# Optimization experiments

Hardware: AMD Instinct MI355X
Metric: run time of the kernel (lower is better)

## Reference

```python
import jax, jax.numpy as jnp
import numpy as np

EPS = 1.1920929e-07  # torch RMSNorm default eps = finfo(float32).eps

def rmsnorm(x, w):
    return x * jax.lax.rsqrt(jnp.mean(x * x, axis=-1, keepdims=True) + EPS) * w

def setup_inputs() -> dict:
    key = jax.random.key(0)
    ks = jax.random.split(key, 12)
    D, H, SC, ST = 1024, 16, 64, 16
    B, T = 2, 2048
    s = 0.02
    return {
        "x": jax.random.normal(ks[0], (B, T, D), jnp.float32),
        "qkv_w": jax.random.normal(ks[1], (3 * D, D), jnp.float32) * s,
        "o_w": jax.random.normal(ks[2], (D, D), jnp.float32) * s,
        "norm1_w": jnp.ones((D,), jnp.float32),
        "norm2_w": jnp.ones((D,), jnp.float32),
        "in_w": jax.random.normal(ks[3], (SC, D), jnp.float32) * s,
        "out_w": jax.random.normal(ks[4], (D, SC), jnp.float32) * s,  # zeros in torch init; randn for nontrivial baseline
        "A_log": jax.random.normal(ks[5], (SC, ST), jnp.float32) * 0.1,
        "Bp_w": jax.random.normal(ks[6], (ST, SC), jnp.float32) * s,
        "Cp_w": jax.random.normal(ks[7], (ST, SC), jnp.float32) * s,
        "dt_w": jax.random.normal(ks[8], (SC, SC), jnp.float32) * s,
        "dt_b": jnp.full((SC,), -3.0, jnp.float32),
        "gate_w": jax.random.normal(ks[9], (SC, D), jnp.float32) * s,
    }

def selective_scan(h, in_w, out_w, A_log, Bp_w, Cp_w, dt_w, dt_b, gate_w):
    B, T, D = h.shape
    SC, ST = A_log.shape
    z = h @ in_w.T                      # [B,T,SC]
    gate = jax.nn.silu(h @ gate_w.T)    # [B,T,SC]
    A = -jnp.exp(A_log)                 # [SC,ST]
    Bi = z @ Bp_w.T                     # [B,T,ST]
    Ci = z @ Cp_w.T                     # [B,T,ST]
    dt = jax.nn.softplus(z @ dt_w.T + dt_b)  # [B,T,SC]
    A_bar = 1.0 + dt[..., None] * A     # [B,T,SC,ST]

    def step(state, inp):
        a_bar, dtz_t, b_t, c_t = inp    # [B,SC,ST],[B,SC],[B,ST],[B,ST]
        state = a_bar * state + dtz_t[:, :, None] * b_t[:, None, :]
        y = jnp.sum(state * c_t[:, None, :], axis=-1)  # [B,SC]
        return state, y

    init = jnp.zeros((B, SC, ST), h.dtype)
    xs = (jnp.swapaxes(A_bar, 0, 1), jnp.swapaxes(dt * z, 0, 1),
          jnp.swapaxes(Bi, 0, 1), jnp.swapaxes(Ci, 0, 1))
    _, ys = jax.lax.scan(step, init, xs)      # [T,B,SC]
    y = jnp.swapaxes(ys, 0, 1) * gate         # [B,T,SC]
    return y @ out_w.T                        # [B,T,D]

def reference(x, qkv_w, o_w, norm1_w, norm2_w, in_w, out_w, A_log, Bp_w, Cp_w, dt_w, dt_b, gate_w):
    B, T, D = x.shape
    H = 16
    hd = D // H
    h = rmsnorm(x, norm1_w)
    qkv = (h @ qkv_w.T).reshape(B, T, 3, H, hd)
    qkv = jnp.transpose(qkv, (2, 0, 3, 1, 4))  # [3,B,H,T,hd]
    q, k, v = qkv[0], qkv[1], qkv[2]
    attn = jnp.einsum('bhqd,bhkd->bhqk', q, k) / np.sqrt(hd).astype(np.float32)
    mask = jnp.tril(jnp.ones((T, T), bool))
    attn = jnp.where(mask, attn, -jnp.inf)
    attn = jax.nn.softmax(attn, axis=-1)
    out = jnp.einsum('bhqk,bhkd->bhqd', attn, v)
    out = jnp.transpose(out, (0, 2, 1, 3)).reshape(B, T, D)
    x = x + out @ o_w.T
    h2 = rmsnorm(x, norm2_w)
    x = x + selective_scan(h2, in_w, out_w, A_log, Bp_w, Cp_w, dt_w, dt_b, gate_w)
    return x
```

## Files before the change

kernel.cpp:

```cpp
#include <hip/hip_runtime.h>
#include <hip/hip_bf16.h>
#include <math.h>

typedef __hip_bfloat16 bf16;
typedef __attribute__((ext_vector_type(4))) float v_f32x4;
typedef __attribute__((ext_vector_type(4))) unsigned short v_u16x4;
typedef __attribute__((ext_vector_type(8))) unsigned short v_u16x8;
typedef __attribute__((ext_vector_type(8))) __bf16 v_bf16x8;
typedef __attribute__((ext_vector_type(4))) __bf16 v_bf16x4;
typedef __attribute__((ext_vector_type(4))) short v_s16x4;

#define NB 2
#define NT 2048
#define ND 1024
#define NH 16
#define NSC 64
#define NST 16
#define NM (NB*NT)
#define RMS_EPS 1.1920929e-07f
#define NCHUNK 32
#define CLEN 64

__device__ inline float b2f(unsigned short u) {
  union { unsigned int i; float f; } v; v.i = ((unsigned int)u) << 16; return v.f;
}
__device__ inline unsigned short f2b(float f) {
  union { float f; unsigned int i; } v; v.f = f;
  unsigned int r = (v.i + 0x7FFF + ((v.i >> 16) & 1)) >> 16;
  return (unsigned short)r;
}

__device__ inline v_f32x4 mfma16(v_bf16x4 a, v_bf16x4 b, v_f32x4 c) {
#if __has_builtin(__builtin_amdgcn_mfma_f32_16x16x16_bf16)
  return __builtin_amdgcn_mfma_f32_16x16x16_bf16(a, b, c, 0, 0, 0);
#else
  union U { v_bf16x4 h; v_s16x4 s; };
  U ua, ub; ua.h = a; ub.h = b;
  return __builtin_amdgcn_mfma_f32_16x16x16bf16_1k(ua.s, ub.s, c, 0, 0, 0);
#endif
}

__device__ inline void gl_lds16(const bf16* g, bf16* l) {
  __builtin_amdgcn_global_load_lds((__attribute__((address_space(1))) void*)g,
                                   (__attribute__((address_space(3))) void*)l,
                                   16, 0, 0);
}

__global__ __launch_bounds__(256) void cvt_rms_kernel(
    const float* __restrict__ qkv_w, const float* __restrict__ o_w,
    const float* __restrict__ out_w, const float* __restrict__ in_w,
    const float* __restrict__ gate_w, const float* __restrict__ dt_w,
    const float* __restrict__ Bp_w, const float* __restrict__ Cp_w,
    bf16* __restrict__ qkvw_b, bf16* __restrict__ ow_b, bf16* __restrict__ outw_b,
    bf16* __restrict__ W1, bf16* __restrict__ W2,
    const float* __restrict__ x, const float* __restrict__ n1w, bf16* __restrict__ h) {
  const int blk = blockIdx.x, t = threadIdx.x;
  if (blk >= 4295) {
    const int row = blk - 4295;
    v_f32x4 xv = *(const v_f32x4*)(x + (size_t)row * ND + t * 4);
    float s = xv[0]*xv[0] + xv[1]*xv[1] + xv[2]*xv[2] + xv[3]*xv[3];
    #pragma unroll
    for (int off = 32; off; off >>= 1) s += __shfl_xor(s, off, 64);
    __shared__ float red[4];
    __shared__ float scale_s;
    if ((t & 63) == 0) red[t >> 6] = s;
    __syncthreads();
    if (t == 0) scale_s = rsqrtf((red[0] + red[1] + red[2] + red[3]) * (1.0f / ND) + RMS_EPS);
    __syncthreads();
    float sc = scale_s;
    v_f32x4 wv = *(const v_f32x4*)(n1w + t * 4);
    v_u16x4 o;
    o[0] = f2b(xv[0] * sc * wv[0]);
    o[1] = f2b(xv[1] * sc * wv[1]);
    o[2] = f2b(xv[2] * sc * wv[2]);
    o[3] = f2b(xv[3] * sc * wv[3]);
    *(v_u16x4*)((unsigned short*)h + (size_t)row * ND + t * 4) = o;
    return;
  }
  const float* src; bf16* dst; int base;
  if (blk < 3072)      { src = qkv_w;  dst = qkvw_b;      base = blk; }
  else if (blk < 4096) { src = o_w;    dst = ow_b;        base = blk - 3072; }
  else if (blk < 4160) { src = out_w;  dst = outw_b;      base = blk - 4096; }
  else if (blk < 4224) { src = in_w;   dst = W1;          base = blk - 4160; }
  else if (blk < 4288) { src = gate_w; dst = W1 + 65536;  base = blk - 4224; }
  else if (blk < 4292) { src = dt_w;   dst = W2;          base = blk - 4288; }
  else if (blk == 4292){ src = Bp_w;   dst = W2 + 4096;   base = 0; }
  else if (blk == 4293){ src = Cp_w;   dst = W2 + 5120;   base = 0; }
  else {
    v_u16x8 z;
    #pragma unroll
    for (int i = 0; i < 8; i++) z[i] = 0;
    *(v_u16x8*)(W2 + 6144 + t * 8) = z;
    return;
  }
  int i = base * 256 + t;
  v_f32x4 v = ((const v_f32x4*)src)[i];
  v_u16x4 o;
  o[0] = f2b(v[0]); o[1] = f2b(v[1]); o[2] = f2b(v[2]); o[3] = f2b(v[3]);
  ((v_u16x4*)dst)[i] = o;
}

template <bool RES, bool OUTF32, bool VT>
__global__ __launch_bounds__(256) void gemm_bt_kernel(
    const bf16* __restrict__ A, const bf16* __restrict__ Bw,
    const float* __restrict__ res, void* __restrict__ Cout, int N, int K, int lda,
    bf16* __restrict__ VtG) {
  __shared__ alignas(16) bf16 As[128 * 32];
  __shared__ alignas(16) bf16 Bs[128 * 32];
  const int tid = threadIdx.x;
  const int wid = tid >> 6;
  const int lane = tid & 63;
  const int c = lane & 15;
  const int quad = lane >> 4;
  const int m0 = blockIdx.y * 128;
  const int n0 = blockIdx.x * 128;
  const int wm = (wid >> 1) * 64;
  const int wn = (wid & 1) * 64;
  const int srow = tid >> 2;
  const int schunk = tid & 3;

  const bf16* Ap0 = A + (size_t)(m0 + srow) * lda + schunk * 8;
  const bf16* Ap1 = Ap0 + (size_t)64 * lda;
  const bf16* Bp0 = Bw + (size_t)(n0 + srow) * K + schunk * 8;
  const bf16* Bp1 = Bp0 + (size_t)64 * K;
  bf16* AsW0 = As + wid * 512;
  bf16* AsW1 = As + 2048 + wid * 512;
  bf16* BsW0 = Bs + wid * 512;
  bf16* BsW1 = Bs + 2048 + wid * 512;

  v_f32x4 acc[4][4];
  #pragma unroll
  for (int i = 0; i < 4; i++)
    #pragma unroll
    for (int j = 0; j < 4; j++)
      #pragma unroll
      for (int r = 0; r < 4; r++) acc[i][j][r] = 0.0f;

  const int nk = K >> 5;
  for (int kt = 0; kt < nk; kt++) {
    gl_lds16(Ap0 + kt * 32, AsW0);
    gl_lds16(Ap1 + kt * 32, AsW1);
    gl_lds16(Bp0 + kt * 32, BsW0);
    gl_lds16(Bp1 + kt * 32, BsW1);
    __syncthreads();
    v_bf16x8 af[4], bfw[4];
    #pragma unroll
    for (int i = 0; i < 4; i++)
      af[i] = *(const v_bf16x8*)&As[(wm + i * 16 + c) * 32 + quad * 8];
    #pragma unroll
    for (int j = 0; j < 4; j++)
      bfw[j] = *(const v_bf16x8*)&Bs[(wn + j * 16 + c) * 32 + quad * 8];
    #pragma unroll
    for (int i = 0; i < 4; i++)
      #pragma unroll
      for (int j = 0; j < 4; j++)
        acc[i][j] = __builtin_amdgcn_mfma_f32_16x16x32_bf16(af[i], bfw[j], acc[i][j], 0, 0, 0);
    __syncthreads();
  }

  if (VT && n0 >= 2048) {
    #pragma unroll
    for (int i = 0; i < 4; i++)
      #pragma unroll
      for (int j = 0; j < 4; j++) {
        int hcol = n0 + wn + j * 16 + c - 2048;
        int hh = hcol >> 6, dd = hcol & 63;
        int rg0 = m0 + wm + i * 16 + quad * 4;
        int bb = rg0 >> 11, t0 = rg0 & (NT - 1);
        v_u16x4 ov;
        #pragma unroll
        for (int r = 0; r < 4; r++) ov[r] = f2b(acc[i][j][r]);
        *(v_u16x4*)((unsigned short*)VtG + ((size_t)((bb * NH + hh) * 64 + dd)) * NT + t0) = ov;
      }
    return;
  }

  #pragma unroll
  for (int i = 0; i < 4; i++)
    #pragma unroll
    for (int j = 0; j < 4; j++)
      #pragma unroll
      for (int r = 0; r < 4; r++) {
        int rg = m0 + wm + i * 16 + quad * 4 + r;
        int cg = n0 + wn + j * 16 + c;
        size_t idx = (size_t)rg * N + cg;
        float v = acc[i][j][r];
        if (RES) v += res[idx];
        if (OUTF32) ((float*)Cout)[idx] = v;
        else ((bf16*)Cout)[idx] = __float2bfloat16(v);
      }
}

template <bool RES, bool OUTF32>
__global__ __launch_bounds__(256) void gemm_bt64_kernel(
    const bf16* __restrict__ A, const bf16* __restrict__ Bw,
    const float* __restrict__ res, void* __restrict__ Cout, int N, int K, int lda) {
  __shared__ alignas(16) bf16 As[64 * 32];
  __shared__ alignas(16) bf16 Bs[128 * 32];
  const int tid = threadIdx.x;
  const int wid = tid >> 6;
  const int lane = tid & 63;
  const int c = lane & 15;
  const int quad = lane >> 4;
  const int m0 = blockIdx.y * 64;
  const int n0 = blockIdx.x * 128;
  const int wm = (wid & 1) * 32;
  const int wn = (wid >> 1) * 64;
  const int srow = tid >> 2;
  const int schunk = tid & 3;

  const bf16* Ap = A + (size_t)(m0 + srow) * lda + schunk * 8;
  const bf16* Bp0 = Bw + (size_t)(n0 + srow) * K + schunk * 8;
  const bf16* Bp1 = Bp0 + (size_t)64 * K;
  bf16* AsW  = As + wid * 512;
  bf16* BsW0 = Bs + wid * 512;
  bf16* BsW1 = Bs + 2048 + wid * 512;

  v_f32x4 acc[2][4];
  #pragma unroll
  for (int i = 0; i < 2; i++)
    #pragma unroll
    for (int j = 0; j < 4; j++)
      #pragma unroll
      for (int r = 0; r < 4; r++) acc[i][j][r] = 0.0f;

  const int nk = K >> 5;
  for (int kt = 0; kt < nk; kt++) {
    gl_lds16(Ap + kt * 32, AsW);
    gl_lds16(Bp0 + kt * 32, BsW0);
    gl_lds16(Bp1 + kt * 32, BsW1);
    __syncthreads();
    v_bf16x8 af[2], bfw[4];
    #pragma unroll
    for (int i = 0; i < 2; i++)
      af[i] = *(const v_bf16x8*)&As[(wm + i * 16 + c) * 32 + quad * 8];
    #pragma unroll
    for (int j = 0; j < 4; j++)
      bfw[j] = *(const v_bf16x8*)&Bs[(wn + j * 16 + c) * 32 + quad * 8];
    #pragma unroll
    for (int i = 0; i < 2; i++)
      #pragma unroll
      for (int j = 0; j < 4; j++)
        acc[i][j] = __builtin_amdgcn_mfma_f32_16x16x32_bf16(af[i], bfw[j], acc[i][j], 0, 0, 0);
    __syncthreads();
  }

  #pragma unroll
  for (int i = 0; i < 2; i++)
    #pragma unroll
    for (int j = 0; j < 4; j++)
      #pragma unroll
      for (int r = 0; r < 4; r++) {
        int rg = m0 + wm + i * 16 + quad * 4 + r;
        int cg = n0 + wn + j * 16 + c;
        size_t idx = (size_t)rg * N + cg;
        float v = acc[i][j][r];
        if (RES) v += res[idx];
        if (OUTF32) ((float*)Cout)[idx] = v;
        else ((bf16*)Cout)[idx] = __float2bfloat16(v);
      }
}

__global__ __launch_bounds__(256) void attn_kernel(const bf16* __restrict__ qkv,
                                                   const bf16* __restrict__ VtG,
                                                   bf16* __restrict__ OP,
                                                   float* __restrict__ L) {
  __shared__ alignas(16) bf16 Qs[64 * 72];
  __shared__ alignas(16) bf16 Ks[64 * 72];
  __shared__ alignas(16) bf16 Vt[64 * 72];
  const int tid = threadIdx.x;
  const int w = tid >> 6;
  const int lane = tid & 63;
  const int c = lane & 15;
  const int quad = lane >> 4;
  const int id = blockIdx.x;
  const int bh = id & 31;
  const int u = id >> 5;
  const int half = u >> 5;
  const int v = u & 31;
  const int j0 = v & 7;
  const int qt = (v & 24) | (((v >> 3) & 1) ? (7 - j0) : j0);
  const int b = bh >> 4;
  const int h = bh & 15;
  const int srow = tid >> 2;
  const int schunk = tid & 3;
  const int n = qt + 1;
  const int nh0 = (n + 1) >> 1;
  const int k0 = half ? nh0 : 0;
  const int k1 = half ? n : nh0;

  {
    const bf16* src = qkv + (size_t)(b * NT + qt * 64 + srow) * 3072 + h * 64 + schunk * 16;
    *(v_u16x8*)&Qs[srow * 72 + schunk * 16] = *(const v_u16x8*)src;
    *(v_u16x8*)&Qs[srow * 72 + schunk * 16 + 8] = *(const v_u16x8*)(src + 8);
  }
  __syncthreads();
  v_bf16x8 aq0 = *(const v_bf16x8*)&Qs[(w * 16 + c) * 72 + quad * 8];
  v_bf16x8 aq1 = *(const v_bf16x8*)&Qs[(w * 16 + c) * 72 + 32 + quad * 8];

  float l_part = 0.0f;
  v_f32x4 o[4];
  #pragma unroll
  for (int jd = 0; jd < 4; jd++)
    #pragma unroll
    for (int r = 0; r < 4; r++) o[jd][r] = 0.0f;

  const int qrow = w * 16 + c;

  for (int kt = k0; kt < k1; kt++) {
    {
      const bf16* ksrc = qkv + (size_t)(b * NT + kt * 64 + srow) * 3072 + 1024 + h * 64 + schunk * 16;
      *(v_u16x8*)&Ks[srow * 72 + schunk * 16] = *(const v_u16x8*)ksrc;
      *(v_u16x8*)&Ks[srow * 72 + schunk * 16 + 8] = *(const v_u16x8*)(ksrc + 8);
      const bf16* vsrc = VtG + (size_t)(bh * 64 + srow) * NT + kt * 64 + schunk * 16;
      *(v_u16x8*)&Vt[srow * 72 + schunk * 16] = *(const v_u16x8*)vsrc;
      *(v_u16x8*)&Vt[srow * 72 + schunk * 16 + 8] = *(const v_u16x8*)(vsrc + 8);
    }
    __syncthreads();

    const bool diag = (kt == qt);
    v_bf16x4 pf[4];
    #pragma unroll
    for (int j = 0; j < 4; j++) {
      v_bf16x8 ak0 = *(const v_bf16x8*)&Ks[(j * 16 + c) * 72 + quad * 8];
      v_bf16x8 ak1 = *(const v_bf16x8*)&Ks[(j * 16 + c) * 72 + 32 + quad * 8];
      v_f32x4 z;
      #pragma unroll
      for (int r = 0; r < 4; r++) z[r] = 0.0f;
      z = __builtin_amdgcn_mfma_f32_16x16x32_bf16(ak0, aq0, z, 0, 0, 0);
      z = __builtin_amdgcn_mfma_f32_16x16x32_bf16(ak1, aq1, z, 0, 0, 0);
      v_u16x4 pu;
      #pragma unroll
      for (int r = 0; r < 4; r++) {
        float p = __expf(z[r] * 0.125f);
        if (diag && (j * 16 + quad * 4 + r) > qrow) p = 0.0f;
        l_part += p;
        pu[r] = f2b(p);
      }
      union { v_u16x4 u; v_bf16x4 h; } cv; cv.u = pu;
      pf[j] = cv.h;
    }
    #pragma unroll
    for (int jd = 0; jd < 4; jd++)
      #pragma unroll
      for (int j = 0; j < 4; j++) {
        v_bf16x4 av = *(const v_bf16x4*)&Vt[(jd * 16 + c) * 72 + j * 16 + quad * 4];
        o[jd] = mfma16(av, pf[j], o[jd]);
      }
    __syncthreads();
  }

  float l = l_part;
  l += __shfl_xor(l, 16, 64);
  l += __shfl_xor(l, 32, 64);

  const size_t ti = (size_t)((bh * 32 + qt) * 2 + half);
  if (quad == 0) L[ti * 64 + qrow] = l;
  unsigned short* OPu = (unsigned short*)OP + (ti * 64 + qrow) * 64;
  #pragma unroll
  for (int jd = 0; jd < 4; jd++) {
    v_u16x4 ov;
    #pragma unroll
    for (int r = 0; r < 4; r++) ov[r] = f2b(o[jd][r]);
    *(v_u16x4*)(OPu + jd * 16 + quad * 4) = ov;
  }
}

__global__ __launch_bounds__(256) void attn_combine_kernel(
    const bf16* __restrict__ OP, const float* __restrict__ L, bf16* __restrict__ out) {
  const int bq = blockIdx.x;
  const int bh = bq >> 5, qt = bq & 31;
  const int b = bh >> 4, h = bh & 15;
  const int tid = threadIdx.x;
  const int q = tid >> 2, dg = (tid & 3) * 16;
  const size_t ti0 = (size_t)bq * 2;
  float inv = 1.0f / (L[ti0 * 64 + q] + L[(ti0 + 1) * 64 + q]);
  const unsigned short* O0 = (const unsigned short*)OP + (ti0 * 64 + q) * 64 + dg;
  const unsigned short* O1 = (const unsigned short*)OP + ((ti0 + 1) * 64 + q) * 64 + dg;
  unsigned short* dst = (unsigned short*)out + (size_t)(b * NT + qt * 64 + q) * ND + h * 64 + dg;
  #pragma unroll
  for (int i = 0; i < 16; i += 4) {
    v_u16x4 a = *(const v_u16x4*)(O0 + i);
    v_u16x4 bb = *(const v_u16x4*)(O1 + i);
    v_u16x4 o;
    #pragma unroll
    for (int r = 0; r < 4; r++) o[r] = f2b((b2f(a[r]) + b2f(bb[r])) * inv);
    *(v_u16x4*)(dst + i) = o;
  }
}

__global__ __launch_bounds__(256) void proj_scan_kernel(
    const float* __restrict__ x1, const float* __restrict__ n2w,
    const bf16* __restrict__ W1, const bf16* __restrict__ W2,
    const float* __restrict__ dt_b,
    float* __restrict__ dt_a, float* __restrict__ dtz_a,
    float* __restrict__ gate_a, float* __restrict__ P2) {
  __shared__ alignas(16) bf16 h2S[16 * 1032];
  __shared__ alignas(16) bf16 Bs[128 * 32];
  __shared__ alignas(16) bf16 zgS[16 * 136];
  const int tid = threadIdx.x;
  const int w = tid >> 6, lane = tid & 63, c = lane & 15, quad = lane >> 4;
  const int m0 = blockIdx.x * 16;
  unsigned short* h2Su = (unsigned short*)h2S;
  unsigned short* zgSu = (unsigned short*)zgS;

  {
    const int r16 = tid >> 4, ct = tid & 15;
    const float* xr = x1 + (size_t)(m0 + r16) * ND + ct * 64;
    v_f32x4 xv[16];
    float ss = 0.0f;
    #pragma unroll
    for (int i = 0; i < 16; i++) {
      xv[i] = *(const v_f32x4*)(xr + i * 4);
      ss += xv[i][0]*xv[i][0] + xv[i][1]*xv[i][1] + xv[i][2]*xv[i][2] + xv[i][3]*xv[i][3];
    }
    ss += __shfl_xor(ss, 1, 64);
    ss += __shfl_xor(ss, 2, 64);
    ss += __shfl_xor(ss, 4, 64);
    ss += __shfl_xor(ss, 8, 64);
    float sc = rsqrtf(ss * (1.0f / ND) + RMS_EPS);
    const float* wr = n2w + ct * 64;
    #pragma unroll
    for (int i = 0; i < 16; i++) {
      v_f32x4 wv = *(const v_f32x4*)(wr + i * 4);
      v_u16x4 o;
      o[0] = f2b(xv[i][0] * sc * wv[0]);
      o[1] = f2b(xv[i][1] * sc * wv[1]);
      o[2] = f2b(xv[i][2] * sc * wv[2]);
      o[3] = f2b(xv[i][3] * sc * wv[3]);
      *(v_u16x4*)&h2Su[r16 * 1032 + ct * 64 + i * 4] = o;
    }
  }
  __syncthreads();

  const int lrow = lane >> 2, lk = lane & 3;
  v_f32x4 acc[2];
  #pragma unroll
  for (int j = 0; j < 2; j++)
    #pragma unroll
    for (int r = 0; r < 4; r++) acc[j][r] = 0.0f;
  for (int kt = 0; kt < 32; kt++) {
    gl_lds16(W1 + (size_t)(w * 32 + lrow) * 1024 + kt * 32 + lk * 8, Bs + (w * 32) * 32);
    gl_lds16(W1 + (size_t)(w * 32 + 16 + lrow) * 1024 + kt * 32 + lk * 8, Bs + (w * 32 + 16) * 32);
    __syncthreads();
    v_bf16x8 af = *(const v_bf16x8*)&h2S[c * 1032 + kt * 32 + quad * 8];
    #pragma unroll
    for (int j = 0; j < 2; j++) {
      v_bf16x8 bfw = *(const v_bf16x8*)&Bs[(w * 32 + j * 16 + c) * 32 + quad * 8];
      acc[j] = __builtin_amdgcn_mfma_f32_16x16x32_bf16(af, bfw, acc[j], 0, 0, 0);
    }
    __syncthreads();
  }
  #pragma unroll
  for (int j = 0; j < 2; j++)
    #pragma unroll
    for (int r = 0; r < 4; r++)
      zgSu[(quad * 4 + r) * 136 + w * 32 + j * 16 + c] = f2b(acc[j][r]);
  __syncthreads();

  v_f32x4 acc2[2];
  #pragma unroll
  for (int j = 0; j < 2; j++)
    #pragma unroll
    for (int r = 0; r < 4; r++) acc2[j][r] = 0.0f;
  for (int kt = 0; kt < 2; kt++) {
    gl_lds16(W2 + (size_t)(w * 32 + lrow) * 64 + kt * 32 + lk * 8, Bs + (w * 32) * 32);
    gl_lds16(W2 + (size_t)(w * 32 + 16 + lrow) * 64 + kt * 32 + lk * 8, Bs + (w * 32 + 16) * 32);
    __syncthreads();
    v_bf16x8 af = *(const v_bf16x8*)&zgS[c * 136 + kt * 32 + quad * 8];
    #pragma unroll
    for (int j = 0; j < 2; j++) {
      v_bf16x8 bfw = *(const v_bf16x8*)&Bs[(w * 32 + j * 16 + c) * 32 + quad * 8];
      acc2[j] = __builtin_amdgcn_mfma_f32_16x16x32_bf16(af, bfw, acc2[j], 0, 0, 0);
    }
    __syncthreads();
  }

  #pragma unroll
  for (int j = 0; j < 2; j++)
    #pragma unroll
    for (int r = 0; r < 4; r++) {
      const int row = quad * 4 + r;
      const int col = w * 32 + j * 16 + c;
      const size_t grow = (size_t)(m0 + row);
      if (w < 2) {
        float z = b2f(zgSu[row * 136 + col]);
        float a = acc2[j][r] + dt_b[col];
        float dt = (a > 20.0f) ? a : log1pf(__expf(a));
        dt_a[grow * NSC + col] = dt;
        dtz_a[grow * NSC + col] = dt * z;
      } else {
        P2[grow * 128 + col] = acc2[j][r];
        float g = b2f(zgSu[row * 136 + col]);
        gate_a[grow * NSC + (col - 64)] = g / (1.0f + __expf(-g));
      }
    }
}

__global__ __launch_bounds__(256) void scanA_kernel(
    const float* __restrict__ dt_a, const float* __restrict__ dtz_a,
    const float* __restrict__ P2, const float* __restrict__ A_log,
    float* __restrict__ Pbuf, float* __restrict__ Sbuf) {
  __shared__ float dtS[CLEN * 16], dtzS[CLEN * 16], biS[CLEN * 16];
  const int k = blockIdx.x, scg = blockIdx.y, b = blockIdx.z;
  const int tid = threadIdx.x;
  const int t0 = k * CLEN;
  {
    int r = tid >> 2, c4 = (tid & 3) * 4;
    *(v_f32x4*)&dtS[r * 16 + c4]  = *(const v_f32x4*)&dt_a[(size_t)(b * NT + t0 + r) * NSC + scg * 16 + c4];
    *(v_f32x4*)&dtzS[r * 16 + c4] = *(const v_f32x4*)&dtz_a[(size_t)(b * NT + t0 + r) * NSC + scg * 16 + c4];
    *(v_f32x4*)&biS[r * 16 + c4]  = *(const v_f32x4*)&P2[(size_t)(b * NT + t0 + r) * 128 + 64 + c4];
  }
  __syncthreads();
  const int st = tid & 15, scl = tid >> 4;
  const float A = -__expf(A_log[(scg * 16 + scl) * NST + st]);
  float P = 1.0f, s = 0.0f;
  #pragma unroll
  for (int t = 0; t < CLEN; t++) {
    float a = fmaf(dtS[t * 16 + scl], A, 1.0f);
    float u = dtzS[t * 16 + scl] * biS[t * 16 + st];
    P *= a;
    s = fmaf(a, s, u);
  }
  size_t idx = (size_t)(b * NCHUNK + k) * 1024 + scg * 256 + tid;
  Pbuf[idx] = P;
  Sbuf[idx] = s;
}

__global__ __launch_bounds__(256) void scanC_kernel(
    const float* __restrict__ dt_a, const float* __restrict__ dtz_a,
    const float* __restrict__ P2, const float* __restrict__ gate_a,
    const float* __restrict__ A_log, const float* __restrict__ Pbuf,
    const float* __restrict__ Sbuf, bf16* __restrict__ ys) {
  __shared__ float dtS[CLEN * 16], dtzS[CLEN * 16], biS[CLEN * 16], ciS[CLEN * 16], gS[CLEN * 16];
  const int k = blockIdx.x, scg = blockIdx.y, b = blockIdx.z;
  const int tid = threadIdx.x;
  const int t0 = k * CLEN;
  {
    int r = tid >> 2, c4 = (tid & 3) * 4;
    *(v_f32x4*)&dtS[r * 16 + c4]  = *(const v_f32x4*)&dt_a[(size_t)(b * NT + t0 + r) * NSC + scg * 16 + c4];
    *(v_f32x4*)&dtzS[r * 16 + c4] = *(const v_f32x4*)&dtz_a[(size_t)(b * NT + t0 + r) * NSC + scg * 16 + c4];
    *(v_f32x4*)&biS[r * 16 + c4]  = *(const v_f32x4*)&P2[(size_t)(b * NT + t0 + r) * 128 + 64 + c4];
    *(v_f32x4*)&ciS[r * 16 + c4]  = *(const v_f32x4*)&P2[(size_t)(b * NT + t0 + r) * 128 + 80 + c4];
    *(v_f32x4*)&gS[r * 16 + c4]   = *(const v_f32x4*)&gate_a[(size_t)(b * NT + t0 + r) * NSC + scg * 16 + c4];
  }
  const int st = tid & 15, scl = tid >> 4;
  const float A = -__expf(A_log[(scg * 16 + scl) * NST + st]);
  float s = 0.0f;
  for (int kk = 0; kk < k; kk++) {
    size_t idx = (size_t)(b * NCHUNK + kk) * 1024 + scg * 256 + tid;
    s = fmaf(Pbuf[idx], s, Sbuf[idx]);
  }
  __syncthreads();
  for (int t = 0; t < CLEN; t++) {
    float a = fmaf(dtS[t * 16 + scl], A, 1.0f);
    float u = dtzS[t * 16 + scl] * biS[t * 16 + st];
    s = fmaf(a, s, u);
    float pv = s * ciS[t * 16 + st];
    pv += __shfl_xor(pv, 1, 64);
    pv += __shfl_xor(pv, 2, 64);
    pv += __shfl_xor(pv, 4, 64);
    pv += __shfl_xor(pv, 8, 64);
    if (st == 0)
      ys[(size_t)(b * NT + t0 + t) * NSC + scg * 16 + scl] = __float2bfloat16(pv * gS[t * 16 + scl]);
  }
}

extern "C" void kernel_launch(void* const* d_in, const int* in_sizes, int n_in,
                              void* d_out, int out_size, void* d_ws, size_t ws_size,
                              hipStream_t stream) {
  const float* x      = (const float*)d_in[0];
  const float* qkv_w  = (const float*)d_in[1];
  const float* o_w    = (const float*)d_in[2];
  const float* n1w    = (const float*)d_in[3];
  const float* n2w    = (const float*)d_in[4];
  const float* in_w   = (const float*)d_in[5];
  const float* out_w  = (const float*)d_in[6];
  const float* A_log  = (const float*)d_in[7];
  const float* Bp_w   = (const float*)d_in[8];
  const float* Cp_w   = (const float*)d_in[9];
  const float* dt_w   = (const float*)d_in[10];
  const float* dt_b   = (const float*)d_in[11];
  const float* gate_w = (const float*)d_in[12];
  float* out = (float*)d_out;

  char* ws = (char*)d_ws;
  size_t off = 0;
  auto alloc = [&](size_t bytes) {
    char* p = ws + off;
    off += (bytes + 255) & ~(size_t)255;
    return p;
  };
  bf16* qkvw_b = (bf16*)alloc((size_t)3 * ND * ND * 2);
  bf16* ow_b   = (bf16*)alloc((size_t)ND * ND * 2);
  bf16* outw_b = (bf16*)alloc((size_t)ND * NSC * 2);
  bf16* W1     = (bf16*)alloc((size_t)128 * ND * 2);
  bf16* W2     = (bf16*)alloc((size_t)128 * NSC * 2);
  char* region0 = alloc((size_t)NM * 3 * ND * 2);
  char* region1 = alloc((size_t)NM * ND * 2);
  bf16* VtG    = (bf16*)alloc((size_t)NB * NH * 64 * NT * 2);
  float* P2    = (float*)alloc((size_t)NM * 128 * 4);
  float* dt_a  = (float*)alloc((size_t)NM * NSC * 4);
  float* dtz_a = (float*)alloc((size_t)NM * NSC * 4);
  float* gate_a= (float*)alloc((size_t)NM * NSC * 4);
  bf16*  ys    = (bf16*)alloc((size_t)NM * NSC * 2);
  float* Pbuf  = (float*)alloc((size_t)NB * NCHUNK * 1024 * 4);
  float* Sbuf  = (float*)alloc((size_t)NB * NCHUNK * 1024 * 4);
  bf16*  OP    = (bf16*)alloc((size_t)2048 * 64 * 64 * 2);
  float* Lb    = (float*)alloc((size_t)2048 * 64 * 4);

  bf16*  qkv     = (bf16*)region0;
  float* x1      = (float*)region0;
  bf16*  h       = (bf16*)region1;
  bf16*  attnout = (bf16*)region1;

  cvt_rms_kernel<<<4295 + NM, 256, 0, stream>>>(qkv_w, o_w, out_w, in_w, gate_w, dt_w,
                                                Bp_w, Cp_w, qkvw_b, ow_b, outw_b, W1, W2,
                                                x, n1w, h);
  gemm_bt_kernel<false, false, true><<<dim3(3 * ND / 128, NM / 128), 256, 0, stream>>>(
      h, qkvw_b, nullptr, (void*)qkv, 3 * ND, ND, ND, VtG);
  attn_kernel<<<2048, 256, 0, stream>>>(qkv, VtG, OP, Lb);
  attn_combine_kernel<<<1024, 256, 0, stream>>>(OP, Lb, attnout);
  gemm_bt64_kernel<true, true><<<dim3(ND / 128, NM / 64), 256, 0, stream>>>(
      attnout, ow_b, x, (void*)x1, ND, ND, ND);
  proj_scan_kernel<<<NM / 16, 256, 0, stream>>>(x1, n2w, W1, W2, dt_b,
                                                dt_a, dtz_a, gate_a, P2);
  scanA_kernel<<<dim3(NCHUNK, 4, NB), 256, 0, stream>>>(dt_a, dtz_a, P2, A_log, Pbuf, Sbuf);
  scanC_kernel<<<dim3(NCHUNK, 4, NB), 256, 0, stream>>>(dt_a, dtz_a, P2, gate_a, A_log,
                                                        Pbuf, Sbuf, ys);
  gemm_bt64_kernel<true, true><<<dim3(ND / 128, NM / 64), 256, 0, stream>>>(
      ys, outw_b, x1, (void*)out, ND, NSC, NSC);
}
```

Baseline: 271.8 us.

## Process two query tiles per attention block to reuse K/V loads

The attention kernel now handles 128 query rows per block, kept as two 64-row groups whose Q fragments stay in registers, so each K/V tile loaded into shared memory serves both groups. The goal is to halve global K/V traffic and the number of blocks. The key range is split in two halves across blocks, and the first group skips tiles beyond its causal limit. The combine kernel and the partial buffers are resized to match. The cost is more registers per thread and fewer blocks (1024), which may reduce occupancy and load balance.

```diff
diff --git a/kernel.cpp b/kernel.cpp
--- a/kernel.cpp
+++ b/kernel.cpp
@@ -265,7 +265,6 @@
                                                    const bf16* __restrict__ VtG,
                                                    bf16* __restrict__ OP,
                                                    float* __restrict__ L) {
-  __shared__ alignas(16) bf16 Qs[64 * 72];
   __shared__ alignas(16) bf16 Ks[64 * 72];
   __shared__ alignas(16) bf16 Vt[64 * 72];
   const int tid = threadIdx.x;
@@ -276,34 +275,42 @@
   const int id = blockIdx.x;
   const int bh = id & 31;
   const int u = id >> 5;
-  const int half = u >> 5;
-  const int v = u & 31;
-  const int j0 = v & 7;
-  const int qt = (v & 24) | (((v >> 3) & 1) ? (7 - j0) : j0);
+  const int half = u >> 4;
+  const int v = u & 15;
+  const int qt2 = (v & 8) ? (15 - (v & 7)) : (v & 7);
   const int b = bh >> 4;
   const int h = bh & 15;
   const int srow = tid >> 2;
   const int schunk = tid & 3;
-  const int n = qt + 1;
-  const int nh0 = (n + 1) >> 1;
-  const int k0 = half ? nh0 : 0;
-  const int k1 = half ? n : nh0;
+  const int qbase = qt2 * 128;
+  const int n = 2 * qt2 + 2;
+  const int k0 = half ? (qt2 + 1) : 0;
+  const int k1 = half ? n : (qt2 + 1);
 
   {
-    const bf16* src = qkv + (size_t)(b * NT + qt * 64 + srow) * 3072 + h * 64 + schunk * 16;
-    *(v_u16x8*)&Qs[srow * 72 + schunk * 16] = *(const v_u16x8*)src;
-    *(v_u16x8*)&Qs[srow * 72 + schunk * 16 + 8] = *(const v_u16x8*)(src + 8);
+    const bf16* s0 = qkv + (size_t)(b * NT + qbase + srow) * 3072 + h * 64 + schunk * 16;
+    *(v_u16x8*)&Ks[srow * 72 + schunk * 16] = *(const v_u16x8*)s0;
+    *(v_u16x8*)&Ks[srow * 72 + schunk * 16 + 8] = *(const v_u16x8*)(s0 + 8);
+    const bf16* s1 = qkv + (size_t)(b * NT + qbase + 64 + srow) * 3072 + h * 64 + schunk * 16;
+    *(v_u16x8*)&Vt[srow * 72 + schunk * 16] = *(const v_u16x8*)s1;
+    *(v_u16x8*)&Vt[srow * 72 + schunk * 16 + 8] = *(const v_u16x8*)(s1 + 8);
   }
   __syncthreads();
-  v_bf16x8 aq0 = *(const v_bf16x8*)&Qs[(w * 16 + c) * 72 + quad * 8];
-  v_bf16x8 aq1 = *(const v_bf16x8*)&Qs[(w * 16 + c) * 72 + 32 + quad * 8];
-
-  float l_part = 0.0f;
-  v_f32x4 o[4];
-  #pragma unroll
-  for (int jd = 0; jd < 4; jd++)
-    #pragma unroll
-    for (int r = 0; r < 4; r++) o[jd][r] = 0.0f;
+  v_bf16x8 aq[2][2];
+  aq[0][0] = *(const v_bf16x8*)&Ks[(w * 16 + c) * 72 + quad * 8];
+  aq[0][1] = *(const v_bf16x8*)&Ks[(w * 16 + c) * 72 + 32 + quad * 8];
+  aq[1][0] = *(const v_bf16x8*)&Vt[(w * 16 + c) * 72 + quad * 8];
+  aq[1][1] = *(const v_bf16x8*)&Vt[(w * 16 + c) * 72 + 32 + quad * 8];
+  __syncthreads();
+
+  float l_part[2] = {0.0f, 0.0f};
+  v_f32x4 o[2][4];
+  #pragma unroll
+  for (int g = 0; g < 2; g++)
+    #pragma unroll
+    for (int jd = 0; jd < 4; jd++)
+      #pragma unroll
+      for (int r = 0; r < 4; r++) o[g][jd][r] = 0.0f;
 
   const int qrow = w * 16 + c;
 
@@ -318,68 +325,93 @@
     }
     __syncthreads();
 
-    const bool diag = (kt == qt);
-    v_bf16x4 pf[4];
+    const bool have0 = (kt <= 2 * qt2);
+    const bool diag0 = (kt == 2 * qt2);
+    const bool diag1 = (kt == 2 * qt2 + 1);
+    v_bf16x4 pf[2][4];
     #pragma unroll
     for (int j = 0; j < 4; j++) {
       v_bf16x8 ak0 = *(const v_bf16x8*)&Ks[(j * 16 + c) * 72 + quad * 8];
       v_bf16x8 ak1 = *(const v_bf16x8*)&Ks[(j * 16 + c) * 72 + 32 + quad * 8];
-      v_f32x4 z;
-      #pragma unroll
-      for (int r = 0; r < 4; r++) z[r] = 0.0f;
-      z = __builtin_amdgcn_mfma_f32_16x16x32_bf16(ak0, aq0, z, 0, 0, 0);
-      z = __builtin_amdgcn_mfma_f32_16x16x32_bf16(ak1, aq1, z, 0, 0, 0);
-      v_u16x4 pu;
-      #pragma unroll
-      for (int r = 0; r < 4; r++) {
-        float p = __expf(z[r] * 0.125f);
-        if (diag && (j * 16 + quad * 4 + r) > qrow) p = 0.0f;
-        l_part += p;
-        pu[r] = f2b(p);
+      if (have0) {
+        v_f32x4 z;
+        #pragma unroll
+        for (int r = 0; r < 4; r++) z[r] = 0.0f;
+        z = __builtin_amdgcn_mfma_f32_16x16x32_bf16(ak0, aq[0][0], z, 0, 0, 0);
+        z = __builtin_amdgcn_mfma_f32_16x16x32_bf16(ak1, aq[0][1], z, 0, 0, 0);
+        v_u16x4 pu;
+        #pragma unroll
+        for (int r = 0; r < 4; r++) {
+          float p = __expf(z[r] * 0.125f);
+          if (diag0 && (j * 16 + quad * 4 + r) > qrow) p = 0.0f;
+          l_part[0] += p;
+          pu[r] = f2b(p);
+        }
+        union { v_u16x4 uu; v_bf16x4 hh; } cv; cv.uu = pu;
+        pf[0][j] = cv.hh;
       }
-      union { v_u16x4 u; v_bf16x4 h; } cv; cv.u = pu;
-      pf[j] = cv.h;
+      {
+        v_f32x4 z;
+        #pragma unroll
+        for (int r = 0; r < 4; r++) z[r] = 0.0f;
+        z = __builtin_amdgcn_mfma_f32_16x16x32_bf16(ak0, aq[1][0], z, 0, 0, 0);
+        z = __builtin_amdgcn_mfma_f32_16x16x32_bf16(ak1, aq[1][1], z, 0, 0, 0);
+        v_u16x4 pu;
+        #pragma unroll
+        for (int r = 0; r < 4; r++) {
+          float p = __expf(z[r] * 0.125f);
+          if (diag1 && (j * 16 + quad * 4 + r) > qrow) p = 0.0f;
+          l_part[1] += p;
+          pu[r] = f2b(p);
+        }
+        union { v_u16x4 uu; v_bf16x4 hh; } cv; cv.uu = pu;
+        pf[1][j] = cv.hh;
+      }
     }
     #pragma unroll
     for (int jd = 0; jd < 4; jd++)
       #pragma unroll
       for (int j = 0; j < 4; j++) {
         v_bf16x4 av = *(const v_bf16x4*)&Vt[(jd * 16 + c) * 72 + j * 16 + quad * 4];
-        o[jd] = mfma16(av, pf[j], o[jd]);
+        if (have0) o[0][jd] = mfma16(av, pf[0][j], o[0][jd]);
+        o[1][jd] = mfma16(av, pf[1][j], o[1][jd]);
       }
     __syncthreads();
   }
 
-  float l = l_part;
-  l += __shfl_xor(l, 16, 64);
-  l += __shfl_xor(l, 32, 64);
-
-  const size_t ti = (size_t)((bh * 32 + qt) * 2 + half);
-  if (quad == 0) L[ti * 64 + qrow] = l;
-  unsigned short* OPu = (unsigned short*)OP + (ti * 64 + qrow) * 64;
-  #pragma unroll
-  for (int jd = 0; jd < 4; jd++) {
-    v_u16x4 ov;
-    #pragma unroll
-    for (int r = 0; r < 4; r++) ov[r] = f2b(o[jd][r]);
-    *(v_u16x4*)(OPu + jd * 16 + quad * 4) = ov;
+  const size_t ti = (size_t)((bh * 16 + qt2) * 2 + half);
+  #pragma unroll
+  for (int g = 0; g < 2; g++) {
+    float l = l_part[g];
+    l += __shfl_xor(l, 16, 64);
+    l += __shfl_xor(l, 32, 64);
+    if (quad == 0) L[ti * 128 + g * 64 + qrow] = l;
+    unsigned short* OPu = (unsigned short*)OP + (ti * 128 + g * 64 + qrow) * 64;
+    #pragma unroll
+    for (int jd = 0; jd < 4; jd++) {
+      v_u16x4 ov;
+      #pragma unroll
+      for (int r = 0; r < 4; r++) ov[r] = f2b(o[g][jd][r]);
+      *(v_u16x4*)(OPu + jd * 16 + quad * 4) = ov;
+    }
   }
 }
 
 __global__ __launch_bounds__(256) void attn_combine_kernel(
     const bf16* __restrict__ OP, const float* __restrict__ L, bf16* __restrict__ out) {
   const int bq = blockIdx.x;
-  const int bh = bq >> 5, qt = bq & 31;
+  const int bh = bq >> 4, qt2 = bq & 15;
   const int b = bh >> 4, h = bh & 15;
   const int tid = threadIdx.x;
-  const int q = tid >> 2, dg = (tid & 3) * 16;
+  const int q = tid >> 1;
+  const int dg = (tid & 1) * 32;
   const size_t ti0 = (size_t)bq * 2;
-  float inv = 1.0f / (L[ti0 * 64 + q] + L[(ti0 + 1) * 64 + q]);
-  const unsigned short* O0 = (const unsigned short*)OP + (ti0 * 64 + q) * 64 + dg;
-  const unsigned short* O1 = (const unsigned short*)OP + ((ti0 + 1) * 64 + q) * 64 + dg;
-  unsigned short* dst = (unsigned short*)out + (size_t)(b * NT + qt * 64 + q) * ND + h * 64 + dg;
-  #pragma unroll
-  for (int i = 0; i < 16; i += 4) {
+  float inv = 1.0f / (L[ti0 * 128 + q] + L[(ti0 + 1) * 128 + q]);
+  const unsigned short* O0 = (const unsigned short*)OP + (ti0 * 128 + q) * 64 + dg;
+  const unsigned short* O1 = (const unsigned short*)OP + ((ti0 + 1) * 128 + q) * 64 + dg;
+  unsigned short* dst = (unsigned short*)out + (size_t)(b * NT + qt2 * 128 + q) * ND + h * 64 + dg;
+  #pragma unroll
+  for (int i = 0; i < 32; i += 4) {
     v_u16x4 a = *(const v_u16x4*)(O0 + i);
     v_u16x4 bb = *(const v_u16x4*)(O1 + i);
     v_u16x4 o;
@@ -606,8 +638,8 @@
   bf16*  ys    = (bf16*)alloc((size_t)NM * NSC * 2);
   float* Pbuf  = (float*)alloc((size_t)NB * NCHUNK * 1024 * 4);
   float* Sbuf  = (float*)alloc((size_t)NB * NCHUNK * 1024 * 4);
-  bf16*  OP    = (bf16*)alloc((size_t)2048 * 64 * 64 * 2);
-  float* Lb    = (float*)alloc((size_t)2048 * 64 * 4);
+  bf16*  OP    = (bf16*)alloc((size_t)1024 * 128 * 64 * 2);
+  float* Lb    = (float*)alloc((size_t)1024 * 128 * 4);
 
   bf16*  qkv     = (bf16*)region0;
   float* x1      = (float*)region0;
@@ -619,8 +651,8 @@
                                                 x, n1w, h);
   gemm_bt_kernel<false, false, true><<<dim3(3 * ND / 128, NM / 128), 256, 0, stream>>>(
       h, qkvw_b, nullptr, (void*)qkv, 3 * ND, ND, ND, VtG);
-  attn_kernel<<<2048, 256, 0, stream>>>(qkv, VtG, OP, Lb);
-  attn_combine_kernel<<<1024, 256, 0, stream>>>(OP, Lb, attnout);
+  attn_kernel<<<1024, 256, 0, stream>>>(qkv, VtG, OP, Lb);
+  attn_combine_kernel<<<512, 256, 0, stream>>>(OP, Lb, attnout);
   gemm_bt64_kernel<true, true><<<dim3(ND / 128, NM / 64), 256, 0, stream>>>(
       attnout, ow_b, x, (void*)x1, ND, ND, ND);
   proj_scan_kernel<<<NM / 16, 256, 0, stream>>>(x1, n2w, W1, W2, dt_b,
```

Measured after the change: 267.7 us. Within noise of the previous version (-1.5%).
